# Kernel tuning notes

Hardware: AMD Instinct MI355X
Metric: run time of the kernel (lower is better)

Reference implementation:

```python
import jax, jax.numpy as jnp
import numpy as np

D_MODEL, N_HEADS = 768, 12
D_K = D_MODEL // N_HEADS
NEG = -1e9


def setup_inputs() -> dict:
    key = jax.random.key(0)
    ks = jax.random.split(key, 12)
    B, S, D = 2, 4096, D_MODEL
    s = 1.0 / np.sqrt(D)
    inp = {
        'query': jax.random.normal(ks[0], (B, S, D), jnp.float32),
        'key': jax.random.normal(ks[1], (B, S, D), jnp.float32),
        'value': jax.random.normal(ks[2], (B, S, D), jnp.float32),
        'mask': jnp.ones((B, S), jnp.int32),
        'Wq': jax.random.normal(ks[3], (D, D), jnp.float32) * s,
        'bq': jnp.zeros((D,), jnp.float32),
        'Wk': jax.random.normal(ks[4], (D, D), jnp.float32) * s,
        'bk': jnp.zeros((D,), jnp.float32),
        'Wv': jax.random.normal(ks[5], (D, D), jnp.float32) * s,
        'bv': jnp.zeros((D,), jnp.float32),
        'Wo': jax.random.normal(ks[6], (D, D), jnp.float32) * s,
        'bo': jnp.zeros((D,), jnp.float32),
    }
    return inp


def reference(query, key, value, mask, Wq, bq, Wk, bk, Wv, bv, Wo, bo):
    B, Sq, D = query.shape
    Sk = key.shape[1]
    # torch Linear: x @ W.T + b; weights stored [out, in]
    def proj(x, W, b, S):
        return (x @ W.T + b).reshape(B, S, N_HEADS, D_K).transpose(0, 2, 1, 3)
    Q = proj(query, Wq, bq, Sq)   # [B,H,Sq,Dk]
    K = proj(key, Wk, bk, Sk)
    V = proj(value, Wv, bv, Sk)
    scores = jnp.einsum('bhqd,bhkd->bhqk', Q, K) / jnp.sqrt(jnp.float32(D_K))
    # padding mask on keys: [B,1,1,Sk]
    scores = jnp.where(mask[:, None, None, :] == 0, NEG, scores)
    # causal mask (triu, diagonal=1)
    causal = jnp.triu(jnp.ones((Sq, Sk), bool), k=1)
    scores = jnp.where(causal[None, None], NEG, scores)
    attn = jax.nn.softmax(scores, axis=-1)
    out = jnp.einsum('bhqk,bhkd->bhqd', attn, V)
    out = out.transpose(0, 2, 1, 3).reshape(B, Sq, D)
    return out @ Wo.T + bo
```

## Files before the change

kernel.cpp:

```cpp
#include <hip/hip_runtime.h>
#include <hip/hip_bf16.h>

#define D_MODEL 768
#define N_HEADS 12
#define D_K     64
#define NEG_INF (-1e9f)
#define KS_PAD  72
#define VT_PAD  136
#define SCALE_Q 0.1803368801111154f
#define W_ELEMS (D_MODEL * D_MODEL)

typedef __attribute__((ext_vector_type(8))) short          bf16x8;
typedef __attribute__((ext_vector_type(4))) float          floatx4;
typedef __attribute__((ext_vector_type(4))) unsigned short ushortx4;
typedef __attribute__((ext_vector_type(2))) unsigned int   uintx2;

static __device__ __forceinline__ unsigned short f2bf(float f) {
    unsigned u = __builtin_bit_cast(unsigned, f);
    u += 0x7FFFu + ((u >> 16) & 1u);
    return (unsigned short)(u >> 16);
}

static __device__ __forceinline__ void gload_lds16(const void* g, void* l) {
    __builtin_amdgcn_global_load_lds(
        (const __attribute__((address_space(1))) void*)g,
        (__attribute__((address_space(3))) void*)l, 16, 0, 0);
}

__global__ __launch_bounds__(256) void convert_w4(
    const float* __restrict__ W0, const float* __restrict__ W1,
    const float* __restrict__ W2, const float* __restrict__ W3,
    unsigned short* __restrict__ out)
{
    const float* src[4] = {W0, W1, W2, W3};
    const float* W = src[blockIdx.y];
    unsigned short* o = out + (size_t)blockIdx.y * W_ELEMS;
    const int i = (blockIdx.x * 256 + threadIdx.x) * 4;
    float4 v = *(const float4*)(W + i);
    ushortx4 h = { f2bf(v.x), f2bf(v.y), f2bf(v.z), f2bf(v.w) };
    *(ushortx4*)(o + i) = h;
}

__global__ __launch_bounds__(256) void convert_a3(
    const float* __restrict__ A0, const float* __restrict__ A1,
    const float* __restrict__ A2,
    unsigned short* __restrict__ O0, unsigned short* __restrict__ O1,
    unsigned short* __restrict__ O2)
{
    const int z = blockIdx.y;
    const float* A = (z == 0) ? A0 : (z == 1) ? A1 : A2;
    unsigned short* O = (z == 0) ? O0 : (z == 1) ? O1 : O2;
    const int i = (blockIdx.x * 256 + threadIdx.x) * 4;
    float4 v = *(const float4*)(A + i);
    ushortx4 h = { f2bf(v.x), f2bf(v.y), f2bf(v.z), f2bf(v.w) };
    *(ushortx4*)(O + i) = h;
}

template <bool QKV>
__global__ __launch_bounds__(256) void gemm128(
    const unsigned short* __restrict__ A0, const unsigned short* __restrict__ A1,
    const unsigned short* __restrict__ A2,
    const unsigned short* __restrict__ W0, const unsigned short* __restrict__ W1,
    const unsigned short* __restrict__ W2,
    const float* __restrict__ b0, const float* __restrict__ b1,
    const float* __restrict__ b2,
    void* __restrict__ C0, void* __restrict__ C1, void* __restrict__ C2,
    int S)
{
    __shared__ __align__(16) unsigned short As[128 * 32];
    __shared__ __align__(16) unsigned short Bs[128 * 32];

    const int z = QKV ? blockIdx.z : 0;
    const unsigned short* A = (z == 0) ? A0 : (z == 1) ? A1 : A2;
    const unsigned short* W = (z == 0) ? W0 : (z == 1) ? W1 : W2;
    const float* bias       = (z == 0) ? b0 : (z == 1) ? b1 : b2;
    void* C                 = (z == 0) ? C0 : (z == 1) ? C1 : C2;
    const float scale = (QKV && z == 0) ? SCALE_Q : 1.0f;
    const int mode = QKV ? ((z == 2) ? 3 : 1) : 0;

    const int tid  = threadIdx.x;
    const int wave = tid >> 6;
    const int lane = tid & 63;
    const int quad = lane >> 4;
    const int l16  = lane & 15;
    const int m0 = blockIdx.x * 128;
    const int n0 = blockIdx.y * 128;
    const int wm = (wave & 1) * 64;
    const int wn = (wave >> 1) * 64;
    const int sr = lane >> 2;
    const int sc = (lane & 3) << 3;

    const floatx4 zero4 = {0.f, 0.f, 0.f, 0.f};
    floatx4 acc[4][4];
    #pragma unroll
    for (int i = 0; i < 4; ++i)
        #pragma unroll
        for (int j = 0; j < 4; ++j) acc[i][j] = zero4;

    for (int k0 = 0; k0 < D_MODEL; k0 += 32) {
        #pragma unroll
        for (int c = 0; c < 2; ++c) {
            const int row = wave * 32 + c * 16;
            gload_lds16(A + (size_t)(m0 + row + sr) * D_MODEL + k0 + sc,
                        As + row * 32);
            gload_lds16(W + (size_t)(n0 + row + sr) * D_MODEL + k0 + sc,
                        Bs + row * 32);
        }
        __syncthreads();

        bf16x8 af[4], bfr[4];
        #pragma unroll
        for (int i = 0; i < 4; ++i)
            af[i] = *(const bf16x8*)(As + (wm + i * 16 + l16) * 32 + quad * 8);
        #pragma unroll
        for (int j = 0; j < 4; ++j)
            bfr[j] = *(const bf16x8*)(Bs + (wn + j * 16 + l16) * 32 + quad * 8);
        #pragma unroll
        for (int i = 0; i < 4; ++i)
            #pragma unroll
            for (int j = 0; j < 4; ++j)
                acc[i][j] = __builtin_amdgcn_mfma_f32_16x16x32_bf16(
                    bfr[j], af[i], acc[i][j], 0, 0, 0);
        __syncthreads();
    }

    #pragma unroll
    for (int i = 0; i < 4; ++i) {
        const int m = m0 + wm + i * 16 + l16;
        #pragma unroll
        for (int j = 0; j < 4; ++j) {
            const int nb = n0 + wn + j * 16 + quad * 4;
            const float4 bv = *(const float4*)(bias + nb);
            float v0 = (acc[i][j][0] + bv.x) * scale;
            float v1 = (acc[i][j][1] + bv.y) * scale;
            float v2 = (acc[i][j][2] + bv.z) * scale;
            float v3 = (acc[i][j][3] + bv.w) * scale;
            if (mode == 0) {
                float4 o = {v0, v1, v2, v3};
                *(float4*)((float*)C + (size_t)m * D_MODEL + nb) = o;
            } else if (mode == 1) {
                ushortx4 o = {f2bf(v0), f2bf(v1), f2bf(v2), f2bf(v3)};
                *(ushortx4*)((unsigned short*)C + (size_t)m * D_MODEL + nb) = o;
            } else {
                const int bb = m / S, s = m - bb * S;
                const int hh = nb >> 6, d = nb & 63;
                unsigned short* base = (unsigned short*)C +
                    ((size_t)(bb * N_HEADS + hh) * D_K + d) * S + s;
                base[0]         = f2bf(v0);
                base[(size_t)S]     = f2bf(v1);
                base[(size_t)S * 2] = f2bf(v2);
                base[(size_t)S * 3] = f2bf(v3);
            }
        }
    }
}

__global__ __launch_bounds__(256) void flash_attn(
    const unsigned short* __restrict__ Qp,
    const unsigned short* __restrict__ Kp,
    const unsigned short* __restrict__ VpT,
    const int* __restrict__ mask,
    unsigned short* __restrict__ O,
    int S)
{
    __shared__ __align__(16) unsigned short Ks [128 * KS_PAD];
    __shared__ __align__(16) unsigned short Vts[64 * VT_PAD];
    __shared__ __align__(16) unsigned short Ps [4][16 * VT_PAD];
    __shared__ __align__(16) float mskf[128];

    const int L  = blockIdx.x;
    const int bh = L % 24;
    const int p  = L / 24;
    const int h  = bh % 12;
    const int b  = bh / 12;
    const int nqt = S >> 6;
    const int tid  = threadIdx.x;
    const int wave = tid >> 6;
    const int lane = tid & 63;
    const int quad = lane >> 4;
    const int l16  = lane & 15;

    const unsigned short* Kbase = Kp  + (size_t)(b * S) * D_MODEL + h * D_K;
    const unsigned short* Vbase = VpT + (size_t)(b * N_HEADS + h) * D_K * S;

    const floatx4 zero4 = {0.f, 0.f, 0.f, 0.f};
    const short one_bf = (short)0x3F80;
    const bf16x8 ones = {one_bf, one_bf, one_bf, one_bf,
                         one_bf, one_bf, one_bf, one_bf};

    #pragma unroll
    for (int sel = 0; sel < 2; ++sel) {
        const int qt = sel ? (nqt - 1 - p) : p;
        const int q0 = qt * 64;
        const int qbase = q0 + wave * 16;
        const int qabs = qbase + l16;

        const size_t rowQ = (size_t)(b * S + qbase + l16) * D_MODEL + h * D_K;
        const bf16x8 qf0 = *(const bf16x8*)(Qp + rowQ + quad * 8);
        const bf16x8 qf1 = *(const bf16x8*)(Qp + rowQ + 32 + quad * 8);

        floatx4 acc2[4];
        floatx4 acc_l = zero4;
        #pragma unroll
        for (int dt = 0; dt < 4; ++dt) acc2[dt] = zero4;

        const int ni = (qt >> 1) + 1;
        for (int kt = 0; kt < ni; ++kt) {
            const int k0 = kt * 128;
            #pragma unroll
            for (int g = tid; g < 1024; g += 256) {
                const int krow = g >> 3, kc = (g & 7) << 3;
                *(bf16x8*)(Ks + krow * KS_PAD + kc) =
                    *(const bf16x8*)(Kbase + (size_t)(k0 + krow) * D_MODEL + kc);
                const int vrow = g >> 4, vc = (g & 15) << 3;
                *(bf16x8*)(Vts + vrow * VT_PAD + vc) =
                    *(const bf16x8*)(Vbase + (size_t)vrow * S + k0 + vc);
            }
            if (tid < 128)
                mskf[tid] = (mask[b * S + k0 + tid] == 0) ? NEG_INF : 0.f;
            __syncthreads();

            floatx4 s[8];
            #pragma unroll
            for (int nt = 0; nt < 8; ++nt) {
                floatx4 c = *(const floatx4*)(mskf + nt * 16 + quad * 4);
                bf16x8 kf0 = *(const bf16x8*)(Ks + (nt * 16 + l16) * KS_PAD + quad * 8);
                bf16x8 kf1 = *(const bf16x8*)(Ks + (nt * 16 + l16) * KS_PAD + 32 + quad * 8);
                c = __builtin_amdgcn_mfma_f32_16x16x32_bf16(kf0, qf0, c, 0, 0, 0);
                c = __builtin_amdgcn_mfma_f32_16x16x32_bf16(kf1, qf1, c, 0, 0, 0);
                s[nt] = c;
            }

            if (kt == ni - 1) {
                #pragma unroll
                for (int nt = 0; nt < 8; ++nt) {
                    const int kb = k0 + nt * 16 + quad * 4;
                    #pragma unroll
                    for (int r = 0; r < 4; ++r)
                        if (kb + r > qabs) s[nt][r] = NEG_INF;
                }
            }

            #pragma unroll
            for (int nt = 0; nt < 8; ++nt) {
                const float e0 = __builtin_exp2f(s[nt][0]);
                const float e1 = __builtin_exp2f(s[nt][1]);
                const float e2 = __builtin_exp2f(s[nt][2]);
                const float e3 = __builtin_exp2f(s[nt][3]);
                uintx2 pk;
                pk[0] = __builtin_amdgcn_perm(__builtin_bit_cast(unsigned, e1),
                                              __builtin_bit_cast(unsigned, e0), 0x07060302u);
                pk[1] = __builtin_amdgcn_perm(__builtin_bit_cast(unsigned, e3),
                                              __builtin_bit_cast(unsigned, e2), 0x07060302u);
                *(uintx2*)(Ps[wave] + l16 * VT_PAD + nt * 16 + quad * 4) = pk;
            }

            #pragma unroll
            for (int kh = 0; kh < 4; ++kh) {
                bf16x8 pf = *(const bf16x8*)(Ps[wave] + l16 * VT_PAD + kh * 32 + quad * 8);
                #pragma unroll
                for (int dt = 0; dt < 4; ++dt) {
                    bf16x8 vf = *(const bf16x8*)(Vts + (dt * 16 + l16) * VT_PAD + kh * 32 + quad * 8);
                    acc2[dt] = __builtin_amdgcn_mfma_f32_16x16x32_bf16(pf, vf, acc2[dt], 0, 0, 0);
                }
                acc_l = __builtin_amdgcn_mfma_f32_16x16x32_bf16(pf, ones, acc_l, 0, 0, 0);
            }
            __syncthreads();
        }

        #pragma unroll
        for (int r = 0; r < 4; ++r) {
            const float inv = 1.f / acc_l[r];
            const int gq = qbase + quad * 4 + r;
            const size_t base = (size_t)(b * S + gq) * D_MODEL + h * D_K;
            #pragma unroll
            for (int dt = 0; dt < 4; ++dt)
                O[base + dt * 16 + l16] = f2bf(acc2[dt][r] * inv);
        }
        __syncthreads();
    }
}

extern "C" void kernel_launch(void* const* d_in, const int* in_sizes, int n_in,
                              void* d_out, int out_size, void* d_ws, size_t ws_size,
                              hipStream_t stream) {
    const float* query = (const float*)d_in[0];
    const float* key   = (const float*)d_in[1];
    const float* value = (const float*)d_in[2];
    const int*   mask  = (const int*)d_in[3];
    const float* Wq = (const float*)d_in[4];
    const float* bq = (const float*)d_in[5];
    const float* Wk = (const float*)d_in[6];
    const float* bk = (const float*)d_in[7];
    const float* Wv = (const float*)d_in[8];
    const float* bv = (const float*)d_in[9];
    const float* Wo = (const float*)d_in[10];
    const float* bo = (const float*)d_in[11];

    const int B  = 2;
    const int BS = in_sizes[3];
    const int S  = BS / B;
    const int M  = BS;

    unsigned short* Qp  = (unsigned short*)d_ws;
    unsigned short* Kp  = Qp  + (size_t)M * D_MODEL;
    unsigned short* VpT = Kp  + (size_t)M * D_MODEL;
    unsigned short* Obf = VpT + (size_t)M * D_MODEL;
    unsigned short* Wbf = Obf + (size_t)M * D_MODEL;
    unsigned short* Wqb = Wbf;
    unsigned short* Wkb = Wbf + (size_t)W_ELEMS;
    unsigned short* Wvb = Wbf + (size_t)W_ELEMS * 2;
    unsigned short* Wob = Wbf + (size_t)W_ELEMS * 3;
    unsigned short* ka = (unsigned short*)d_out;
    unsigned short* va = ka + (size_t)M * D_MODEL;

    dim3 blk(256);
    convert_w4<<<dim3(W_ELEMS / 1024, 4), blk, 0, stream>>>(Wq, Wk, Wv, Wo, Wbf);
    convert_a3<<<dim3((M * D_MODEL) / 1024, 3), blk, 0, stream>>>(
        query, key, value, Obf, ka, va);

    gemm128<true><<<dim3(M / 128, D_MODEL / 128, 3), blk, 0, stream>>>(
        Obf, ka, va, Wqb, Wkb, Wvb, bq, bk, bv, Qp, Kp, VpT, S);

    flash_attn<<<768, blk, 0, stream>>>(Qp, Kp, VpT, mask, Obf, S);

    gemm128<false><<<dim3(M / 128, D_MODEL / 128, 1), blk, 0, stream>>>(
        Obf, Obf, Obf, Wob, Wob, Wob, bo, bo, bo,
        d_out, d_out, d_out, S);
}
```

Baseline: 319.6 us.

## Split flash attention key tiles across waves with cross-wave reduction epilogue

Reworks the attention kernel so each wave owns a 32-key slice of each 128-key tile and computes all 64 queries, loading K and V fragments directly from global memory into registers instead of staging them in shared memory. This removes the per-tile block-wide barriers and shared-memory staging of K/V. Waves whose key slice lies fully beyond the causal limit skip work. Partial outputs and row sums are then combined through a shared-memory tree reduction. It trades more register pressure (16 accumulators per wave, occupancy hint of 3) and uncoalesced direct global loads for fewer synchronisations.

```diff
diff --git a/kernel.cpp b/kernel.cpp
--- a/kernel.cpp
+++ b/kernel.cpp
@@ -5,10 +5,10 @@
 #define N_HEADS 12
 #define D_K     64
 #define NEG_INF (-1e9f)
-#define KS_PAD  72
-#define VT_PAD  136
 #define SCALE_Q 0.1803368801111154f
 #define W_ELEMS (D_MODEL * D_MODEL)
+#define PS_PAD  40
+#define RED_PAD 68
 
 typedef __attribute__((ext_vector_type(8))) short          bf16x8;
 typedef __attribute__((ext_vector_type(4))) float          floatx4;
@@ -146,7 +146,7 @@
                 const int hh = nb >> 6, d = nb & 63;
                 unsigned short* base = (unsigned short*)C +
                     ((size_t)(bb * N_HEADS + hh) * D_K + d) * S + s;
-                base[0]         = f2bf(v0);
+                base[0]             = f2bf(v0);
                 base[(size_t)S]     = f2bf(v1);
                 base[(size_t)S * 2] = f2bf(v2);
                 base[(size_t)S * 3] = f2bf(v3);
@@ -155,7 +155,12 @@
     }
 }
 
-__global__ __launch_bounds__(256) void flash_attn(
+union FlashSmem {
+    unsigned short Ps[4][64 * PS_PAD];
+    struct { float red[2][64 * RED_PAD]; float redl[2][64]; } ep;
+};
+
+__global__ __launch_bounds__(256, 3) void flash_attn(
     const unsigned short* __restrict__ Qp,
     const unsigned short* __restrict__ Kp,
     const unsigned short* __restrict__ VpT,
@@ -163,10 +168,7 @@
     unsigned short* __restrict__ O,
     int S)
 {
-    __shared__ __align__(16) unsigned short Ks [128 * KS_PAD];
-    __shared__ __align__(16) unsigned short Vts[64 * VT_PAD];
-    __shared__ __align__(16) unsigned short Ps [4][16 * VT_PAD];
-    __shared__ __align__(16) float mskf[128];
+    __shared__ __align__(16) FlashSmem sm;
 
     const int L  = blockIdx.x;
     const int bh = L % 24;
@@ -179,9 +181,12 @@
     const int lane = tid & 63;
     const int quad = lane >> 4;
     const int l16  = lane & 15;
+    const int ksl  = wave * 32;
 
     const unsigned short* Kbase = Kp  + (size_t)(b * S) * D_MODEL + h * D_K;
     const unsigned short* Vbase = VpT + (size_t)(b * N_HEADS + h) * D_K * S;
+    const int* maskb = mask + b * S;
+    unsigned short* Psw = sm.Ps[wave];
 
     const floatx4 zero4 = {0.f, 0.f, 0.f, 0.f};
     const short one_bf = (short)0x3F80;
@@ -192,90 +197,142 @@
     for (int sel = 0; sel < 2; ++sel) {
         const int qt = sel ? (nqt - 1 - p) : p;
         const int q0 = qt * 64;
-        const int qbase = q0 + wave * 16;
-        const int qabs = qbase + l16;
-
-        const size_t rowQ = (size_t)(b * S + qbase + l16) * D_MODEL + h * D_K;
-        const bf16x8 qf0 = *(const bf16x8*)(Qp + rowQ + quad * 8);
-        const bf16x8 qf1 = *(const bf16x8*)(Qp + rowQ + 32 + quad * 8);
-
-        floatx4 acc2[4];
-        floatx4 acc_l = zero4;
-        #pragma unroll
-        for (int dt = 0; dt < 4; ++dt) acc2[dt] = zero4;
+
+        bf16x8 qf[4][2];
+        #pragma unroll
+        for (int qg = 0; qg < 4; ++qg) {
+            const size_t rowQ = (size_t)(b * S + q0 + qg * 16 + l16) * D_MODEL + h * D_K;
+            qf[qg][0] = *(const bf16x8*)(Qp + rowQ + quad * 8);
+            qf[qg][1] = *(const bf16x8*)(Qp + rowQ + 32 + quad * 8);
+        }
+
+        floatx4 acc2[4][4];
+        floatx4 acc_l[4];
+        #pragma unroll
+        for (int qg = 0; qg < 4; ++qg) {
+            acc_l[qg] = zero4;
+            #pragma unroll
+            for (int dt = 0; dt < 4; ++dt) acc2[qg][dt] = zero4;
+        }
 
         const int ni = (qt >> 1) + 1;
         for (int kt = 0; kt < ni; ++kt) {
-            const int k0 = kt * 128;
-            #pragma unroll
-            for (int g = tid; g < 1024; g += 256) {
-                const int krow = g >> 3, kc = (g & 7) << 3;
-                *(bf16x8*)(Ks + krow * KS_PAD + kc) =
-                    *(const bf16x8*)(Kbase + (size_t)(k0 + krow) * D_MODEL + kc);
-                const int vrow = g >> 4, vc = (g & 15) << 3;
-                *(bf16x8*)(Vts + vrow * VT_PAD + vc) =
-                    *(const bf16x8*)(Vbase + (size_t)vrow * S + k0 + vc);
-            }
-            if (tid < 128)
-                mskf[tid] = (mask[b * S + k0 + tid] == 0) ? NEG_INF : 0.f;
-            __syncthreads();
-
-            floatx4 s[8];
-            #pragma unroll
-            for (int nt = 0; nt < 8; ++nt) {
-                floatx4 c = *(const floatx4*)(mskf + nt * 16 + quad * 4);
-                bf16x8 kf0 = *(const bf16x8*)(Ks + (nt * 16 + l16) * KS_PAD + quad * 8);
-                bf16x8 kf1 = *(const bf16x8*)(Ks + (nt * 16 + l16) * KS_PAD + 32 + quad * 8);
-                c = __builtin_amdgcn_mfma_f32_16x16x32_bf16(kf0, qf0, c, 0, 0, 0);
-                c = __builtin_amdgcn_mfma_f32_16x16x32_bf16(kf1, qf1, c, 0, 0, 0);
-                s[nt] = c;
-            }
-
-            if (kt == ni - 1) {
-                #pragma unroll
-                for (int nt = 0; nt < 8; ++nt) {
-                    const int kb = k0 + nt * 16 + quad * 4;
+            const int kb = kt * 128 + ksl;
+            if (kb > q0 + 63) continue;
+            const bool last = (kt == ni - 1);
+
+            bf16x8 kf[2][2];
+            #pragma unroll
+            for (int ntg = 0; ntg < 2; ++ntg) {
+                const size_t rowK = (size_t)(kb + ntg * 16 + l16) * D_MODEL;
+                kf[ntg][0] = *(const bf16x8*)(Kbase + rowK + quad * 8);
+                kf[ntg][1] = *(const bf16x8*)(Kbase + rowK + 32 + quad * 8);
+            }
+            bf16x8 vf[4];
+            #pragma unroll
+            for (int dt = 0; dt < 4; ++dt)
+                vf[dt] = *(const bf16x8*)(Vbase + (size_t)(dt * 16 + l16) * S + kb + quad * 8);
+
+            #pragma unroll
+            for (int ntg = 0; ntg < 2; ++ntg) {
+                const int4 mv = *(const int4*)(maskb + kb + ntg * 16 + quad * 4);
+                floatx4 minit;
+                minit[0] = (mv.x == 0) ? NEG_INF : 0.f;
+                minit[1] = (mv.y == 0) ? NEG_INF : 0.f;
+                minit[2] = (mv.z == 0) ? NEG_INF : 0.f;
+                minit[3] = (mv.w == 0) ? NEG_INF : 0.f;
+
+                #pragma unroll
+                for (int qg = 0; qg < 4; ++qg) {
+                    floatx4 c = minit;
+                    c = __builtin_amdgcn_mfma_f32_16x16x32_bf16(kf[ntg][0], qf[qg][0], c, 0, 0, 0);
+                    c = __builtin_amdgcn_mfma_f32_16x16x32_bf16(kf[ntg][1], qf[qg][1], c, 0, 0, 0);
+                    if (last) {
+                        const int kk = kb + ntg * 16 + quad * 4;
+                        const int qq = q0 + qg * 16 + l16;
+                        #pragma unroll
+                        for (int r = 0; r < 4; ++r)
+                            if (kk + r > qq) c[r] = NEG_INF;
+                    }
+                    const float e0 = __builtin_exp2f(c[0]);
+                    const float e1 = __builtin_exp2f(c[1]);
+                    const float e2 = __builtin_exp2f(c[2]);
+                    const float e3 = __builtin_exp2f(c[3]);
+                    uintx2 pk;
+                    pk[0] = __builtin_amdgcn_perm(__builtin_bit_cast(unsigned, e1),
+                                                  __builtin_bit_cast(unsigned, e0), 0x07060302u);
+                    pk[1] = __builtin_amdgcn_perm(__builtin_bit_cast(unsigned, e3),
+                                                  __builtin_bit_cast(unsigned, e2), 0x07060302u);
+                    *(uintx2*)(Psw + (qg * 16 + l16) * PS_PAD + ntg * 16 + quad * 4) = pk;
+                }
+            }
+
+            #pragma unroll
+            for (int qg = 0; qg < 4; ++qg) {
+                const bf16x8 pf = *(const bf16x8*)(Psw + (qg * 16 + l16) * PS_PAD + quad * 8);
+                #pragma unroll
+                for (int dt = 0; dt < 4; ++dt)
+                    acc2[qg][dt] = __builtin_amdgcn_mfma_f32_16x16x32_bf16(
+                        pf, vf[dt], acc2[qg][dt], 0, 0, 0);
+                acc_l[qg] = __builtin_amdgcn_mfma_f32_16x16x32_bf16(
+                    pf, ones, acc_l[qg], 0, 0, 0);
+            }
+        }
+
+        __syncthreads();
+        if (wave >= 2) {
+            float* rb = sm.ep.red[wave - 2];
+            #pragma unroll
+            for (int qg = 0; qg < 4; ++qg) {
+                #pragma unroll
+                for (int dt = 0; dt < 4; ++dt)
+                    *(floatx4*)(rb + (dt * 16 + l16) * RED_PAD + qg * 16 + quad * 4) = acc2[qg][dt];
+                if (l16 == 0)
+                    *(floatx4*)(sm.ep.redl[wave - 2] + qg * 16 + quad * 4) = acc_l[qg];
+            }
+        }
+        __syncthreads();
+        if (wave < 2) {
+            const float* rb = sm.ep.red[wave];
+            #pragma unroll
+            for (int qg = 0; qg < 4; ++qg) {
+                #pragma unroll
+                for (int dt = 0; dt < 4; ++dt)
+                    acc2[qg][dt] += *(const floatx4*)(rb + (dt * 16 + l16) * RED_PAD + qg * 16 + quad * 4);
+                acc_l[qg] += *(const floatx4*)(sm.ep.redl[wave] + qg * 16 + quad * 4);
+            }
+        }
+        __syncthreads();
+        if (wave == 1) {
+            float* rb = sm.ep.red[0];
+            #pragma unroll
+            for (int qg = 0; qg < 4; ++qg) {
+                #pragma unroll
+                for (int dt = 0; dt < 4; ++dt)
+                    *(floatx4*)(rb + (dt * 16 + l16) * RED_PAD + qg * 16 + quad * 4) = acc2[qg][dt];
+                if (l16 == 0)
+                    *(floatx4*)(sm.ep.redl[0] + qg * 16 + quad * 4) = acc_l[qg];
+            }
+        }
+        __syncthreads();
+        if (wave == 0) {
+            const float* rb = sm.ep.red[0];
+            #pragma unroll
+            for (int qg = 0; qg < 4; ++qg) {
+                acc_l[qg] += *(const floatx4*)(sm.ep.redl[0] + qg * 16 + quad * 4);
+                #pragma unroll
+                for (int dt = 0; dt < 4; ++dt)
+                    acc2[qg][dt] += *(const floatx4*)(rb + (dt * 16 + l16) * RED_PAD + qg * 16 + quad * 4);
+                #pragma unroll
+                for (int r = 0; r < 4; ++r) {
+                    const float inv = 1.f / acc_l[qg][r];
+                    const int gq = q0 + qg * 16 + quad * 4 + r;
+                    unsigned short* ob = O + (size_t)(b * S + gq) * D_MODEL + h * D_K;
                     #pragma unroll
-                    for (int r = 0; r < 4; ++r)
-                        if (kb + r > qabs) s[nt][r] = NEG_INF;
+                    for (int dt = 0; dt < 4; ++dt)
+                        ob[dt * 16 + l16] = f2bf(acc2[qg][dt][r] * inv);
                 }
             }
-
-            #pragma unroll
-            for (int nt = 0; nt < 8; ++nt) {
-                const float e0 = __builtin_exp2f(s[nt][0]);
-                const float e1 = __builtin_exp2f(s[nt][1]);
-                const float e2 = __builtin_exp2f(s[nt][2]);
-                const float e3 = __builtin_exp2f(s[nt][3]);
-                uintx2 pk;
-                pk[0] = __builtin_amdgcn_perm(__builtin_bit_cast(unsigned, e1),
-                                              __builtin_bit_cast(unsigned, e0), 0x07060302u);
-                pk[1] = __builtin_amdgcn_perm(__builtin_bit_cast(unsigned, e3),
-                                              __builtin_bit_cast(unsigned, e2), 0x07060302u);
-                *(uintx2*)(Ps[wave] + l16 * VT_PAD + nt * 16 + quad * 4) = pk;
-            }
-
-            #pragma unroll
-            for (int kh = 0; kh < 4; ++kh) {
-                bf16x8 pf = *(const bf16x8*)(Ps[wave] + l16 * VT_PAD + kh * 32 + quad * 8);
-                #pragma unroll
-                for (int dt = 0; dt < 4; ++dt) {
-                    bf16x8 vf = *(const bf16x8*)(Vts + (dt * 16 + l16) * VT_PAD + kh * 32 + quad * 8);
-                    acc2[dt] = __builtin_amdgcn_mfma_f32_16x16x32_bf16(pf, vf, acc2[dt], 0, 0, 0);
-                }
-                acc_l = __builtin_amdgcn_mfma_f32_16x16x32_bf16(pf, ones, acc_l, 0, 0, 0);
-            }
-            __syncthreads();
-        }
-
-        #pragma unroll
-        for (int r = 0; r < 4; ++r) {
-            const float inv = 1.f / acc_l[r];
-            const int gq = qbase + quad * 4 + r;
-            const size_t base = (size_t)(b * S + gq) * D_MODEL + h * D_K;
-            #pragma unroll
-            for (int dt = 0; dt < 4; ++dt)
-                O[base + dt * 16 + l16] = f2bf(acc2[dt][r] * inv);
         }
         __syncthreads();
     }
```

Result: slower. 380.6 us (+19.1%).

## Split flash attention waves across query and key halves with LDS reduction

Applied to the files above, without the earlier changes.

Reorganizes the flash-attention block so each wave handles 32 queries over one 64-key half instead of 16 queries over all 128 keys, and reuses each K/V fragment for two query groups. The two key halves are combined at the end through a shared-memory reduction. K/V tiles are now loaded with direct global-to-LDS loads in an MFMA-fragment-friendly layout rather than through registers with padded rows. Fully masked key halves are skipped. Launch bounds now request 3 blocks per CU. The extra reduction and barrier add epilogue cost, and the occupancy hint may force register spills.

```diff
diff --git a/kernel.cpp b/kernel.cpp
--- a/kernel.cpp
+++ b/kernel.cpp
@@ -5,10 +5,10 @@
 #define N_HEADS 12
 #define D_K     64
 #define NEG_INF (-1e9f)
-#define KS_PAD  72
-#define VT_PAD  136
 #define SCALE_Q 0.1803368801111154f
 #define W_ELEMS (D_MODEL * D_MODEL)
+#define PS_PAD  72
+#define RED_PAD 36
 
 typedef __attribute__((ext_vector_type(8))) short          bf16x8;
 typedef __attribute__((ext_vector_type(4))) float          floatx4;
@@ -146,7 +146,7 @@
                 const int hh = nb >> 6, d = nb & 63;
                 unsigned short* base = (unsigned short*)C +
                     ((size_t)(bb * N_HEADS + hh) * D_K + d) * S + s;
-                base[0]         = f2bf(v0);
+                base[0]             = f2bf(v0);
                 base[(size_t)S]     = f2bf(v1);
                 base[(size_t)S * 2] = f2bf(v2);
                 base[(size_t)S * 3] = f2bf(v3);
@@ -155,7 +155,18 @@
     }
 }
 
-__global__ __launch_bounds__(256) void flash_attn(
+union FlashSmem {
+    struct {
+        unsigned short KsF[16 * 512];
+        unsigned short VtsF[16 * 512];
+    } kv;
+    struct {
+        float red[2][64 * RED_PAD];
+        float redl[2][32];
+    } ep;
+};
+
+__global__ __launch_bounds__(256, 3) void flash_attn(
     const unsigned short* __restrict__ Qp,
     const unsigned short* __restrict__ Kp,
     const unsigned short* __restrict__ VpT,
@@ -163,9 +174,8 @@
     unsigned short* __restrict__ O,
     int S)
 {
-    __shared__ __align__(16) unsigned short Ks [128 * KS_PAD];
-    __shared__ __align__(16) unsigned short Vts[64 * VT_PAD];
-    __shared__ __align__(16) unsigned short Ps [4][16 * VT_PAD];
+    __shared__ __align__(16) FlashSmem sm;
+    __shared__ __align__(16) unsigned short Ps[4][32 * PS_PAD];
     __shared__ __align__(16) float mskf[128];
 
     const int L  = blockIdx.x;
@@ -176,12 +186,16 @@
     const int nqt = S >> 6;
     const int tid  = threadIdx.x;
     const int wave = tid >> 6;
+    const int qw   = wave & 1;
+    const int kw   = wave >> 1;
     const int lane = tid & 63;
     const int quad = lane >> 4;
     const int l16  = lane & 15;
+    const int ksl  = kw * 64;
 
     const unsigned short* Kbase = Kp  + (size_t)(b * S) * D_MODEL + h * D_K;
     const unsigned short* Vbase = VpT + (size_t)(b * N_HEADS + h) * D_K * S;
+    unsigned short* Psw = Ps[wave];
 
     const floatx4 zero4 = {0.f, 0.f, 0.f, 0.f};
     const short one_bf = (short)0x3F80;
@@ -192,90 +206,132 @@
     for (int sel = 0; sel < 2; ++sel) {
         const int qt = sel ? (nqt - 1 - p) : p;
         const int q0 = qt * 64;
-        const int qbase = q0 + wave * 16;
-        const int qabs = qbase + l16;
-
-        const size_t rowQ = (size_t)(b * S + qbase + l16) * D_MODEL + h * D_K;
-        const bf16x8 qf0 = *(const bf16x8*)(Qp + rowQ + quad * 8);
-        const bf16x8 qf1 = *(const bf16x8*)(Qp + rowQ + 32 + quad * 8);
-
-        floatx4 acc2[4];
-        floatx4 acc_l = zero4;
-        #pragma unroll
-        for (int dt = 0; dt < 4; ++dt) acc2[dt] = zero4;
+        const int qs = q0 + qw * 32;
+
+        bf16x8 qf[2][2];
+        #pragma unroll
+        for (int qg = 0; qg < 2; ++qg) {
+            const size_t rowQ = (size_t)(b * S + qs + qg * 16 + l16) * D_MODEL + h * D_K;
+            qf[qg][0] = *(const bf16x8*)(Qp + rowQ + quad * 8);
+            qf[qg][1] = *(const bf16x8*)(Qp + rowQ + 32 + quad * 8);
+        }
+
+        floatx4 accO[2][4];
+        floatx4 accL[2];
+        #pragma unroll
+        for (int qg = 0; qg < 2; ++qg) {
+            accL[qg] = zero4;
+            #pragma unroll
+            for (int dt = 0; dt < 4; ++dt) accO[qg][dt] = zero4;
+        }
 
         const int ni = (qt >> 1) + 1;
         for (int kt = 0; kt < ni; ++kt) {
             const int k0 = kt * 128;
             #pragma unroll
-            for (int g = tid; g < 1024; g += 256) {
-                const int krow = g >> 3, kc = (g & 7) << 3;
-                *(bf16x8*)(Ks + krow * KS_PAD + kc) =
-                    *(const bf16x8*)(Kbase + (size_t)(k0 + krow) * D_MODEL + kc);
-                const int vrow = g >> 4, vc = (g & 15) << 3;
-                *(bf16x8*)(Vts + vrow * VT_PAD + vc) =
-                    *(const bf16x8*)(Vbase + (size_t)vrow * S + k0 + vc);
+            for (int c = 0; c < 4; ++c) {
+                const int kg = wave * 2 + (c >> 1);
+                const int kh = c & 1;
+                gload_lds16(Kbase + (size_t)(k0 + kg * 16 + l16) * D_MODEL + kh * 32 + quad * 8,
+                            sm.kv.KsF + (kg * 2 + kh) * 512);
+                const int dt = wave;
+                const int kq = c;
+                gload_lds16(Vbase + (size_t)(dt * 16 + l16) * S + k0 + kq * 32 + quad * 8,
+                            sm.kv.VtsF + (dt * 4 + kq) * 512);
             }
             if (tid < 128)
                 mskf[tid] = (mask[b * S + k0 + tid] == 0) ? NEG_INF : 0.f;
             __syncthreads();
 
-            floatx4 s[8];
-            #pragma unroll
-            for (int nt = 0; nt < 8; ++nt) {
-                floatx4 c = *(const floatx4*)(mskf + nt * 16 + quad * 4);
-                bf16x8 kf0 = *(const bf16x8*)(Ks + (nt * 16 + l16) * KS_PAD + quad * 8);
-                bf16x8 kf1 = *(const bf16x8*)(Ks + (nt * 16 + l16) * KS_PAD + 32 + quad * 8);
-                c = __builtin_amdgcn_mfma_f32_16x16x32_bf16(kf0, qf0, c, 0, 0, 0);
-                c = __builtin_amdgcn_mfma_f32_16x16x32_bf16(kf1, qf1, c, 0, 0, 0);
-                s[nt] = c;
-            }
-
-            if (kt == ni - 1) {
-                #pragma unroll
-                for (int nt = 0; nt < 8; ++nt) {
-                    const int kb = k0 + nt * 16 + quad * 4;
-                    #pragma unroll
-                    for (int r = 0; r < 4; ++r)
-                        if (kb + r > qabs) s[nt][r] = NEG_INF;
+            const int kb = k0 + ksl;
+            if (kb <= q0 + 63) {
+                const bool diag = (kb + 63 > qs);
+
+                #pragma unroll
+                for (int nt = 0; nt < 4; ++nt) {
+                    const floatx4 minit = *(const floatx4*)(mskf + ksl + nt * 16 + quad * 4);
+                    const int kgf = (kw * 4 + nt) * 2;
+                    const bf16x8 kf0 = *(const bf16x8*)(sm.kv.KsF + kgf * 512 + lane * 8);
+                    const bf16x8 kf1 = *(const bf16x8*)(sm.kv.KsF + (kgf + 1) * 512 + lane * 8);
+                    #pragma unroll
+                    for (int qg = 0; qg < 2; ++qg) {
+                        floatx4 c = minit;
+                        c = __builtin_amdgcn_mfma_f32_16x16x32_bf16(kf0, qf[qg][0], c, 0, 0, 0);
+                        c = __builtin_amdgcn_mfma_f32_16x16x32_bf16(kf1, qf[qg][1], c, 0, 0, 0);
+                        if (diag) {
+                            const int kk = kb + nt * 16 + quad * 4;
+                            const int qq = qs + qg * 16 + l16;
+                            #pragma unroll
+                            for (int r = 0; r < 4; ++r)
+                                if (kk + r > qq) c[r] = NEG_INF;
+                        }
+                        const float e0 = __builtin_exp2f(c[0]);
+                        const float e1 = __builtin_exp2f(c[1]);
+                        const float e2 = __builtin_exp2f(c[2]);
+                        const float e3 = __builtin_exp2f(c[3]);
+                        uintx2 pk;
+                        pk[0] = __builtin_amdgcn_perm(__builtin_bit_cast(unsigned, e1),
+                                                      __builtin_bit_cast(unsigned, e0), 0x07060302u);
+                        pk[1] = __builtin_amdgcn_perm(__builtin_bit_cast(unsigned, e3),
+                                                      __builtin_bit_cast(unsigned, e2), 0x07060302u);
+                        *(uintx2*)(Psw + (qg * 16 + l16) * PS_PAD + nt * 16 + quad * 4) = pk;
+                    }
                 }
-            }
-
-            #pragma unroll
-            for (int nt = 0; nt < 8; ++nt) {
-                const float e0 = __builtin_exp2f(s[nt][0]);
-                const float e1 = __builtin_exp2f(s[nt][1]);
-                const float e2 = __builtin_exp2f(s[nt][2]);
-                const float e3 = __builtin_exp2f(s[nt][3]);
-                uintx2 pk;
-                pk[0] = __builtin_amdgcn_perm(__builtin_bit_cast(unsigned, e1),
-                                              __builtin_bit_cast(unsigned, e0), 0x07060302u);
-                pk[1] = __builtin_amdgcn_perm(__builtin_bit_cast(unsigned, e3),
-                                              __builtin_bit_cast(unsigned, e2), 0x07060302u);
-                *(uintx2*)(Ps[wave] + l16 * VT_PAD + nt * 16 + quad * 4) = pk;
-            }
-
-            #pragma unroll
-            for (int kh = 0; kh < 4; ++kh) {
-                bf16x8 pf = *(const bf16x8*)(Ps[wave] + l16 * VT_PAD + kh * 32 + quad * 8);
-                #pragma unroll
-                for (int dt = 0; dt < 4; ++dt) {
-                    bf16x8 vf = *(const bf16x8*)(Vts + (dt * 16 + l16) * VT_PAD + kh * 32 + quad * 8);
-                    acc2[dt] = __builtin_amdgcn_mfma_f32_16x16x32_bf16(pf, vf, acc2[dt], 0, 0, 0);
+
+                #pragma unroll
+                for (int kh = 0; kh < 2; ++kh) {
+                    bf16x8 pf[2];
+                    #pragma unroll
+                    for (int qg = 0; qg < 2; ++qg)
+                        pf[qg] = *(const bf16x8*)(Psw + (qg * 16 + l16) * PS_PAD + kh * 32 + quad * 8);
+                    #pragma unroll
+                    for (int dt = 0; dt < 4; ++dt) {
+                        const bf16x8 vf = *(const bf16x8*)(
+                            sm.kv.VtsF + (dt * 4 + kw * 2 + kh) * 512 + lane * 8);
+                        #pragma unroll
+                        for (int qg = 0; qg < 2; ++qg)
+                            accO[qg][dt] = __builtin_amdgcn_mfma_f32_16x16x32_bf16(
+                                pf[qg], vf, accO[qg][dt], 0, 0, 0);
+                    }
+                    #pragma unroll
+                    for (int qg = 0; qg < 2; ++qg)
+                        accL[qg] = __builtin_amdgcn_mfma_f32_16x16x32_bf16(
+                            pf[qg], ones, accL[qg], 0, 0, 0);
                 }
-                acc_l = __builtin_amdgcn_mfma_f32_16x16x32_bf16(pf, ones, acc_l, 0, 0, 0);
             }
             __syncthreads();
         }
 
-        #pragma unroll
-        for (int r = 0; r < 4; ++r) {
-            const float inv = 1.f / acc_l[r];
-            const int gq = qbase + quad * 4 + r;
-            const size_t base = (size_t)(b * S + gq) * D_MODEL + h * D_K;
-            #pragma unroll
-            for (int dt = 0; dt < 4; ++dt)
-                O[base + dt * 16 + l16] = f2bf(acc2[dt][r] * inv);
+        if (kw == 1) {
+            float* rb = sm.ep.red[qw];
+            #pragma unroll
+            for (int qg = 0; qg < 2; ++qg) {
+                #pragma unroll
+                for (int dt = 0; dt < 4; ++dt)
+                    *(floatx4*)(rb + (dt * 16 + l16) * RED_PAD + qg * 16 + quad * 4) = accO[qg][dt];
+                if (l16 == 0)
+                    *(floatx4*)(sm.ep.redl[qw] + qg * 16 + quad * 4) = accL[qg];
+            }
+        }
+        __syncthreads();
+        if (kw == 0) {
+            const float* rb = sm.ep.red[qw];
+            #pragma unroll
+            for (int qg = 0; qg < 2; ++qg) {
+                accL[qg] += *(const floatx4*)(sm.ep.redl[qw] + qg * 16 + quad * 4);
+                #pragma unroll
+                for (int dt = 0; dt < 4; ++dt)
+                    accO[qg][dt] += *(const floatx4*)(rb + (dt * 16 + l16) * RED_PAD + qg * 16 + quad * 4);
+                #pragma unroll
+                for (int r = 0; r < 4; ++r) {
+                    const float inv = 1.f / accL[qg][r];
+                    const int gq = qs + qg * 16 + quad * 4 + r;
+                    unsigned short* ob = O + (size_t)(b * S + gq) * D_MODEL + h * D_K;
+                    #pragma unroll
+                    for (int dt = 0; dt < 4; ++dt)
+                        ob[dt * 16 + l16] = f2bf(accO[qg][dt][r] * inv);
+                }
+            }
         }
         __syncthreads();
     }
```

Result: no change. 320.8 us (+0.4%).
